# Performance work log

Hardware: AMD Instinct MI355X
Metric: run time of the kernel (lower is better)

Reference implementation:

```python
import jax, jax.numpy as jnp
import numpy as np

N, E, D, H = 50000, 800000, 128, 4
C = D // H  # per-head out channels
NEG_SLOPE = 0.2
BN_EPS = 1e-5


def _glorot(key, shape, fan):
    return jax.random.normal(key, shape, jnp.float32) / np.sqrt(fan)


def setup_inputs() -> dict:
    key = jax.random.key(0)
    ks = jax.random.split(key, 8)
    inp = {
        'x': jax.random.normal(ks[0], (N, D), jnp.float32),
        'edge_index': jax.random.randint(ks[1], (2, E), 0, N, dtype=jnp.int32),
        'Wl1': _glorot(ks[2], (D, D), D), 'Wr1': _glorot(ks[3], (D, D), D),
        'att1': _glorot(ks[4], (H, C), C), 'b1': jnp.zeros((D,), jnp.float32),
        'gamma1': jnp.ones((D,), jnp.float32), 'beta1': jnp.zeros((D,), jnp.float32),
        'Wl2': _glorot(ks[5], (D, D), D), 'Wr2': _glorot(ks[6], (D, D), D),
        'att2': _glorot(ks[7], (H, C), C), 'b2': jnp.zeros((D,), jnp.float32),
        'gamma2': jnp.ones((D,), jnp.float32), 'beta2': jnp.zeros((D,), jnp.float32),
    }
    return inp


def gatv2_conv(x, src, dst, Wl, Wr, att, bias):
    # PyG GATv2Conv, concat=True, add_self_loops handled by caller.
    n = x.shape[0]
    xl = (x @ Wl).reshape(n, H, C)  # source-side transform
    xr = (x @ Wr).reshape(n, H, C)  # target-side transform
    e = xl[src] + xr[dst]                      # [E', H, C]
    e = jnp.where(e > 0, e, NEG_SLOPE * e)     # LeakyReLU
    logits = jnp.einsum('ehc,hc->eh', e, att)  # [E', H]
    # segment softmax over destination node
    m = jax.ops.segment_max(logits, dst, num_segments=n)  # [N, H]
    ex = jnp.exp(logits - m[dst])
    den = jax.ops.segment_sum(ex, dst, num_segments=n)
    alpha = ex / den[dst]                      # [E', H]
    out = jax.ops.segment_sum(alpha[:, :, None] * xl[src], dst, num_segments=n)
    return out.reshape(n, H * C) + bias


def batchnorm(x, gamma, beta):
    mu = x.mean(0)
    var = x.var(0)
    return gamma * (x - mu) * jax.lax.rsqrt(var + BN_EPS) + beta


def reference(x, edge_index, Wl1, Wr1, att1, b1, gamma1, beta1,
              Wl2, Wr2, att2, b2, gamma2, beta2):
    n = x.shape[0]
    loop = jnp.arange(n, dtype=edge_index.dtype)
    src = jnp.concatenate([edge_index[0], loop])  # add self-loops (PyG default)
    dst = jnp.concatenate([edge_index[1], loop])
    identity = x
    out = gatv2_conv(x, src, dst, Wl1, Wr1, att1, b1)
    out = jax.nn.relu(batchnorm(out, gamma1, beta1))
    out = gatv2_conv(out, src, dst, Wl2, Wr2, att2, b2)
    out = batchnorm(out, gamma2, beta2) + identity
    return jax.nn.relu(out)
```

## Files before the change

kernel.cpp:

```cpp
#include <hip/hip_runtime.h>
#include <cstdint>
#include <cstddef>

#define D 128
#define BN_EPS 1e-5f
#define NEG_INF -3.0e38f
#define BN_BLOCKS 512

typedef __attribute__((ext_vector_type(8))) short bf16x8;
typedef __attribute__((ext_vector_type(4))) float f32x4;

static __device__ __forceinline__ unsigned short f2bf(float f) {
    uint32_t u = __float_as_uint(f);
    uint32_t r = (u + 0x7fffu + ((u >> 16) & 1u)) >> 16;
    return (unsigned short)r;
}

static __device__ __forceinline__ float qsum4(float x) {
    x += __int_as_float(__builtin_amdgcn_update_dpp(0, __float_as_int(x), 0xB1, 0xF, 0xF, true));
    x += __int_as_float(__builtin_amdgcn_update_dpp(0, __float_as_int(x), 0x4E, 0xF, 0xF, true));
    return x;
}

__global__ void zero_kernel(int* cnt, int n, unsigned short* esrc_tail) {
    int i = blockIdx.x * 256 + threadIdx.x;
    if (i < n) cnt[i] = 0;
    if (i < 16) esrc_tail[i] = 0;
}

__global__ void hist_kernel(const int* __restrict__ dst, int* __restrict__ cnt, int E) {
    int e = blockIdx.x * 256 + threadIdx.x;
    if (e < E) atomicAdd(&cnt[dst[e]], 1);
}

__global__ void scan_block(const int* __restrict__ cnt, int* __restrict__ row_start,
                           int* __restrict__ bsum, int n) {
    __shared__ int tmp[256];
    int tid = threadIdx.x;
    int i = blockIdx.x * 256 + tid;
    int v = (i < n) ? cnt[i] : 0;
    tmp[tid] = v; __syncthreads();
    for (int off = 1; off < 256; off <<= 1) {
        int t = (tid >= off) ? tmp[tid - off] : 0;
        __syncthreads();
        tmp[tid] += t; __syncthreads();
    }
    if (i < n) row_start[i + 1] = tmp[tid];
    if (tid == 255) bsum[blockIdx.x] = tmp[255];
}

__global__ void scan_bsum(int* bsum, int nb) {
    __shared__ int tmp[256];
    int tid = threadIdx.x;
    int v = (tid < nb) ? bsum[tid] : 0;
    tmp[tid] = v; __syncthreads();
    for (int off = 1; off < 256; off <<= 1) {
        int t = (tid >= off) ? tmp[tid - off] : 0;
        __syncthreads();
        tmp[tid] += t; __syncthreads();
    }
    if (tid < nb) bsum[tid] = tmp[tid];
}

__global__ void scan_fix(int* __restrict__ row_start, const int* __restrict__ bsum,
                         int* __restrict__ cursor, int n) {
    int i = blockIdx.x * 256 + threadIdx.x;
    if (i < n) {
        int add = (blockIdx.x > 0) ? bsum[blockIdx.x - 1] : 0;
        int val = row_start[i + 1] + add;
        row_start[i + 1] = val;
        if (i + 1 < n) cursor[i + 1] = val;
    }
    if (i == 0) { row_start[0] = 0; cursor[0] = 0; }
}

__global__ void scatter_kernel(const int* __restrict__ src, const int* __restrict__ dst,
                               int* __restrict__ cursor, unsigned short* __restrict__ esrc, int E) {
    int e = blockIdx.x * 256 + threadIdx.x;
    if (e < E) {
        int p = atomicAdd(&cursor[dst[e]], 1);
        esrc[p] = (unsigned short)src[e];
    }
}

__global__ void repack_w(const float* __restrict__ Wl, const float* __restrict__ Wr,
                         unsigned short* __restrict__ Bp) {
    int idx = blockIdx.x * 256 + threadIdx.x;
    int i    = idx & 7;
    int lane = (idx >> 3) & 63;
    int kt   = (idx >> 9) & 3;
    int jt   = idx >> 11;
    int k   = kt * 32 + (lane >> 4) * 8 + i;
    int col = jt * 16 + (lane & 15);
    float v = (col < 128) ? Wl[k * 128 + col] : Wr[k * 128 + (col - 128)];
    Bp[idx] = f2bf(v);
}

template<bool BN>
__global__ __launch_bounds__(256, 2) void gemm_mfma(
    const float* __restrict__ X, const unsigned short* __restrict__ Bp,
    const float* __restrict__ scale, const float* __restrict__ shift,
    unsigned short* __restrict__ xl, float* __restrict__ xr, int n)
{
    __shared__ unsigned short smem[32768];
    {
        const float4* s = (const float4*)Bp;
        float4* d = (float4*)smem;
        #pragma unroll
        for (int it = 0; it < 16; ++it)
            d[it * 256 + threadIdx.x] = s[it * 256 + threadIdx.x];
    }
    __syncthreads();

    int wid = threadIdx.x >> 6, lane = threadIdx.x & 63;
    int nw = (n + 31) >> 5;
    int wrow = blockIdx.x * 4 + wid;
    if (wrow >= nw) return;
    int r0 = wrow * 32;
    int m = lane & 15, hi = lane >> 4;

    f32x4 accA[16], accB[16];
    #pragma unroll
    for (int jt = 0; jt < 16; ++jt) {
        accA[jt] = (f32x4){0.f, 0.f, 0.f, 0.f};
        accB[jt] = (f32x4){0.f, 0.f, 0.f, 0.f};
    }

    int rA = r0 + m;      if (rA > n - 1) rA = n - 1;
    int rB = r0 + 16 + m; if (rB > n - 1) rB = n - 1;
    const float* xrowA = X + (size_t)rA * D;
    const float* xrowB = X + (size_t)rB * D;

    #pragma unroll
    for (int kt = 0; kt < 4; ++kt) {
        int kb = kt * 32 + hi * 8;
        float sca[8], shf[8];
        if (BN) {
            float4 s0 = *(const float4*)(scale + kb);
            float4 s1 = *(const float4*)(scale + kb + 4);
            float4 h0 = *(const float4*)(shift + kb);
            float4 h1 = *(const float4*)(shift + kb + 4);
            sca[0]=s0.x; sca[1]=s0.y; sca[2]=s0.z; sca[3]=s0.w;
            sca[4]=s1.x; sca[5]=s1.y; sca[6]=s1.z; sca[7]=s1.w;
            shf[0]=h0.x; shf[1]=h0.y; shf[2]=h0.z; shf[3]=h0.w;
            shf[4]=h1.x; shf[5]=h1.y; shf[6]=h1.z; shf[7]=h1.w;
        }
        float4 a0 = *(const float4*)(xrowA + kb);
        float4 a1 = *(const float4*)(xrowA + kb + 4);
        float4 b0 = *(const float4*)(xrowB + kb);
        float4 b1 = *(const float4*)(xrowB + kb + 4);
        float avA[8] = {a0.x, a0.y, a0.z, a0.w, a1.x, a1.y, a1.z, a1.w};
        float avB[8] = {b0.x, b0.y, b0.z, b0.w, b1.x, b1.y, b1.z, b1.w};
        bf16x8 afragA, afragB;
        #pragma unroll
        for (int i = 0; i < 8; ++i) {
            float va = avA[i], vb = avB[i];
            if (BN) {
                va = fmaxf(va * sca[i] + shf[i], 0.f);
                vb = fmaxf(vb * sca[i] + shf[i], 0.f);
            }
            afragA[i] = (short)f2bf(va);
            afragB[i] = (short)f2bf(vb);
        }
        #pragma unroll
        for (int jt = 0; jt < 16; ++jt) {
            bf16x8 bfrag = *(const bf16x8*)(smem + (size_t)((jt * 4 + kt) * 64 + lane) * 8);
            accA[jt] = __builtin_amdgcn_mfma_f32_16x16x32_bf16(afragA, bfrag, accA[jt], 0, 0, 0);
            accB[jt] = __builtin_amdgcn_mfma_f32_16x16x32_bf16(afragB, bfrag, accB[jt], 0, 0, 0);
        }
    }

    #pragma unroll
    for (int jt = 0; jt < 16; ++jt) {
        int col = jt * 16 + m;
        #pragma unroll
        for (int r = 0; r < 4; ++r) {
            int rowA = r0 + hi * 4 + r;
            int rowB = rowA + 16;
            if (rowA < n) {
                float v = accA[jt][r];
                if (jt < 8) xl[(size_t)rowA * D + col] = f2bf(v);
                else        xr[(size_t)rowA * D + (col - 128)] = v;
            }
            if (rowB < n) {
                float v = accB[jt][r];
                if (jt < 8) xl[(size_t)rowB * D + col] = f2bf(v);
                else        xr[(size_t)rowB * D + (col - 128)] = v;
            }
        }
    }
}

__global__ __launch_bounds__(256) void gat_kernel(
    const unsigned short* __restrict__ xl, const float* __restrict__ xr,
    const float* __restrict__ att, const float* __restrict__ bias,
    const int* __restrict__ row_start, const unsigned short* __restrict__ esrc,
    float* __restrict__ h, int n)
{
    const float L2E = 1.44269504089f;
    int wid = threadIdx.x >> 6;
    int lane = threadIdx.x & 63;
    int v = blockIdx.x * 4 + wid;
    if (v >= n) return;
    int g  = lane >> 4;
    int il = lane & 15;

    float xrv[8], av[8];
    {
        float4 xa = *(const float4*)(xr + (size_t)v * D + il * 8);
        float4 xb = *(const float4*)(xr + (size_t)v * D + il * 8 + 4);
        xrv[0]=xa.x; xrv[1]=xa.y; xrv[2]=xa.z; xrv[3]=xa.w;
        xrv[4]=xb.x; xrv[5]=xb.y; xrv[6]=xb.z; xrv[7]=xb.w;
        float4 aa = *(const float4*)(att + il * 8);
        float4 ab = *(const float4*)(att + il * 8 + 4);
        av[0]=aa.x*L2E; av[1]=aa.y*L2E; av[2]=aa.z*L2E; av[3]=aa.w*L2E;
        av[4]=ab.x*L2E; av[5]=ab.y*L2E; av[6]=ab.z*L2E; av[7]=ab.w*L2E;
    }

    int p = row_start[v];
    int deg = row_start[v + 1] - p;
    int vcnt = deg + 1;

    float m = NEG_INF, den = 0.f;
    float acc[8] = {0.f, 0.f, 0.f, 0.f, 0.f, 0.f, 0.f, 0.f};

    auto unpack = [](uint4 q, float* x) {
        x[0] = __uint_as_float(q.x << 16); x[1] = __uint_as_float(q.x & 0xffff0000u);
        x[2] = __uint_as_float(q.y << 16); x[3] = __uint_as_float(q.y & 0xffff0000u);
        x[4] = __uint_as_float(q.z << 16); x[5] = __uint_as_float(q.z & 0xffff0000u);
        x[6] = __uint_as_float(q.w << 16); x[7] = __uint_as_float(q.w & 0xffff0000u);
    };
    auto logit = [&](const float* x) {
        float d = 0.f;
        #pragma unroll
        for (int k = 0; k < 8; ++k) {
            float f = x[k] + xrv[k];
            f = fmaxf(f, 0.2f * f);
            d = fmaf(av[k], f, d);
        }
        return qsum4(d);
    };

    {
        uint32_t u0 = (g == 0) ? (uint32_t)v : (uint32_t)esrc[p + g - 1];
        bool val0 = g < vcnt;
        uint4 q0 = *(const uint4*)(xl + ((size_t)u0 << 7) + il * 8);
        float x[8]; unpack(q0, x);
        float lg = val0 ? logit(x) : NEG_INF;
        if (__any(lg > m + 8.f)) { m = fmaxf(m, lg); }
        float pex = val0 ? exp2f(lg - m) : 0.f;
        den += pex;
        #pragma unroll
        for (int k = 0; k < 8; ++k) acc[k] = fmaf(pex, x[k], acc[k]);
    }
    for (int base = 4; base < vcnt; base += 8) {
        int iA = base + g, iB = base + 4 + g;
        bool vA = iA < vcnt, vB = iB < vcnt;
        uint32_t uA = vA ? (uint32_t)esrc[p + iA - 1] : 0u;
        uint32_t uB = vB ? (uint32_t)esrc[p + iB - 1] : 0u;
        uint4 qA = *(const uint4*)(xl + ((size_t)uA << 7) + il * 8);
        uint4 qB = *(const uint4*)(xl + ((size_t)uB << 7) + il * 8);
        float xA[8], xB[8];
        unpack(qA, xA); unpack(qB, xB);
        float lgA = logit(xA); lgA = vA ? lgA : NEG_INF;
        float lgB = logit(xB); lgB = vB ? lgB : NEG_INF;
        float mx = fmaxf(lgA, lgB);
        if (__any(mx > m + 8.f)) {
            float nm = fmaxf(m, mx);
            float sc = exp2f(m - nm);
            den *= sc;
            #pragma unroll
            for (int k = 0; k < 8; ++k) acc[k] *= sc;
            m = nm;
        }
        float pA = exp2f(lgA - m);
        float pB = exp2f(lgB - m);
        den += pA + pB;
        #pragma unroll
        for (int k = 0; k < 8; ++k)
            acc[k] = fmaf(pA, xA[k], fmaf(pB, xB[k], acc[k]));
    }

    float m2 = fmaxf(m, __shfl_xor(m, 16));
    float M  = fmaxf(m2, __shfl_xor(m2, 32));
    float sc = exp2f(m - M);
    den *= sc;
    den += __shfl_xor(den, 16);
    den += __shfl_xor(den, 32);
    #pragma unroll
    for (int k = 0; k < 8; ++k) {
        acc[k] *= sc;
        acc[k] += __shfl_xor(acc[k], 16);
        acc[k] += __shfl_xor(acc[k], 32);
    }
    if (g == 0) {
        float inv = 1.f / den;
        float4 ba = *(const float4*)(bias + il * 8);
        float4 bb = *(const float4*)(bias + il * 8 + 4);
        float4 o0, o1;
        o0.x = fmaf(acc[0], inv, ba.x); o0.y = fmaf(acc[1], inv, ba.y);
        o0.z = fmaf(acc[2], inv, ba.z); o0.w = fmaf(acc[3], inv, ba.w);
        o1.x = fmaf(acc[4], inv, bb.x); o1.y = fmaf(acc[5], inv, bb.y);
        o1.z = fmaf(acc[6], inv, bb.z); o1.w = fmaf(acc[7], inv, bb.w);
        *(float4*)(h + (size_t)v * D + il * 8)     = o0;
        *(float4*)(h + (size_t)v * D + il * 8 + 4) = o1;
    }
}

__global__ __launch_bounds__(256) void bn_stats(const float* __restrict__ h,
                                                float* __restrict__ psum, float* __restrict__ psum2, int n)
{
    int c4 = threadIdx.x & 31;
    int ty = threadIdx.x >> 5;
    float sx = 0.f, sy = 0.f, sz = 0.f, sw = 0.f;
    float qx = 0.f, qy = 0.f, qz = 0.f, qw = 0.f;
    for (int r = blockIdx.x * 8 + ty; r < n; r += gridDim.x * 8) {
        float4 v = *(const float4*)(h + (size_t)r * D + c4 * 4);
        sx += v.x; sy += v.y; sz += v.z; sw += v.w;
        qx = fmaf(v.x, v.x, qx); qy = fmaf(v.y, v.y, qy);
        qz = fmaf(v.z, v.z, qz); qw = fmaf(v.w, v.w, qw);
    }
    __shared__ float4 smA[256], smB[256];
    smA[threadIdx.x] = make_float4(sx, sy, sz, sw);
    smB[threadIdx.x] = make_float4(qx, qy, qz, qw);
    __syncthreads();
    #pragma unroll
    for (int off = 128; off >= 32; off >>= 1) {
        if (threadIdx.x < off) {
            float4 a = smA[threadIdx.x], b = smA[threadIdx.x + off];
            smA[threadIdx.x] = make_float4(a.x + b.x, a.y + b.y, a.z + b.z, a.w + b.w);
            float4 c = smB[threadIdx.x], d2 = smB[threadIdx.x + off];
            smB[threadIdx.x] = make_float4(c.x + d2.x, c.y + d2.y, c.z + d2.z, c.w + d2.w);
        }
        __syncthreads();
    }
    if (threadIdx.x < 32) {
        ((float4*)psum)[blockIdx.x * 32 + threadIdx.x]  = smA[threadIdx.x];
        ((float4*)psum2)[blockIdx.x * 32 + threadIdx.x] = smB[threadIdx.x];
    }
}

__global__ __launch_bounds__(256) void bn_mid(const float* __restrict__ psum, const float* __restrict__ psum2,
                                              float* __restrict__ pmid, float* __restrict__ pmid2)
{
    int c4 = threadIdx.x & 31;
    int rg = threadIdx.x >> 5;
    float4 s = make_float4(0.f, 0.f, 0.f, 0.f), q = make_float4(0.f, 0.f, 0.f, 0.f);
    #pragma unroll
    for (int k = 0; k < 4; ++k) {
        int r = blockIdx.x * 32 + rg + k * 8;
        float4 a = ((const float4*)psum)[r * 32 + c4];
        float4 b = ((const float4*)psum2)[r * 32 + c4];
        s.x += a.x; s.y += a.y; s.z += a.z; s.w += a.w;
        q.x += b.x; q.y += b.y; q.z += b.z; q.w += b.w;
    }
    __shared__ float4 smA[256], smB[256];
    smA[threadIdx.x] = s; smB[threadIdx.x] = q;
    __syncthreads();
    #pragma unroll
    for (int off = 128; off >= 32; off >>= 1) {
        if (threadIdx.x < off) {
            float4 a = smA[threadIdx.x], b = smA[threadIdx.x + off];
            smA[threadIdx.x] = make_float4(a.x + b.x, a.y + b.y, a.z + b.z, a.w + b.w);
            float4 c = smB[threadIdx.x], d2 = smB[threadIdx.x + off];
            smB[threadIdx.x] = make_float4(c.x + d2.x, c.y + d2.y, c.z + d2.z, c.w + d2.w);
        }
        __syncthreads();
    }
    if (threadIdx.x < 32) {
        ((float4*)pmid)[blockIdx.x * 32 + threadIdx.x]  = smA[threadIdx.x];
        ((float4*)pmid2)[blockIdx.x * 32 + threadIdx.x] = smB[threadIdx.x];
    }
}

__global__ void bn_final(const float* __restrict__ psum, const float* __restrict__ psum2,
                         const float* __restrict__ gamma, const float* __restrict__ beta,
                         float* __restrict__ scale, float* __restrict__ shift,
                         float inv_n, int nblk)
{
    int c = threadIdx.x & 127;
    int half = threadIdx.x >> 7;
    float s = 0.f, s2 = 0.f;
    for (int b = half; b < nblk; b += 2) {
        s  += psum[b * 128 + c];
        s2 += psum2[b * 128 + c];
    }
    __shared__ float sm[256], sm2[256];
    sm[threadIdx.x] = s; sm2[threadIdx.x] = s2; __syncthreads();
    if (half == 0) {
        s  += sm[threadIdx.x + 128];
        s2 += sm2[threadIdx.x + 128];
        float mu = s * inv_n;
        float var = s2 * inv_n - mu * mu;
        float inv = rsqrtf(var + BN_EPS);
        float sc = gamma[c] * inv;
        scale[c] = sc;
        shift[c] = beta[c] - mu * sc;
    }
}

__global__ __launch_bounds__(256) void final_kernel(
    const float* __restrict__ h2, const float* __restrict__ x,
    const float* __restrict__ scale, const float* __restrict__ shift,
    float* __restrict__ out, int total)
{
    int i = blockIdx.x * 256 + threadIdx.x;
    if (i * 4 >= total) return;
    float4 hv = ((const float4*)h2)[i];
    float4 xv = ((const float4*)x)[i];
    int c = (i * 4) & 127;
    float4 o;
    o.x = fmaxf(hv.x * scale[c + 0] + shift[c + 0] + xv.x, 0.f);
    o.y = fmaxf(hv.y * scale[c + 1] + shift[c + 1] + xv.y, 0.f);
    o.z = fmaxf(hv.z * scale[c + 2] + shift[c + 2] + xv.z, 0.f);
    o.w = fmaxf(hv.w * scale[c + 3] + shift[c + 3] + xv.w, 0.f);
    ((float4*)out)[i] = o;
}

extern "C" void kernel_launch(void* const* d_in, const int* in_sizes, int n_in,
                              void* d_out, int out_size, void* d_ws, size_t ws_size,
                              hipStream_t stream)
{
    const float* x    = (const float*)d_in[0];
    const int*   ei   = (const int*)  d_in[1];
    const float* Wl1  = (const float*)d_in[2];
    const float* Wr1  = (const float*)d_in[3];
    const float* att1 = (const float*)d_in[4];
    const float* b1   = (const float*)d_in[5];
    const float* g1   = (const float*)d_in[6];
    const float* be1  = (const float*)d_in[7];
    const float* Wl2  = (const float*)d_in[8];
    const float* Wr2  = (const float*)d_in[9];
    const float* att2 = (const float*)d_in[10];
    const float* b2   = (const float*)d_in[11];
    const float* g2   = (const float*)d_in[12];
    const float* be2  = (const float*)d_in[13];
    float* out = (float*)d_out;

    int n = in_sizes[0] / D;
    int E = in_sizes[1] / 2;
    const int* e_src = ei;
    const int* e_dst = ei + E;

    char* w = (char*)d_ws;
    auto alloc = [&](size_t bytes) -> char* {
        char* p = w;
        w += (bytes + 255) / 256 * 256;
        return p;
    };
    unsigned short* xl = (unsigned short*)alloc((size_t)n * D * 2);
    float* xr          = (float*)alloc((size_t)n * D * 4);
    float* h           = (float*)alloc((size_t)n * D * 4);
    int* row_start     = (int*)alloc((size_t)(n + 1) * 4);
    int* cnt           = (int*)alloc((size_t)n * 4);
    int* cursor        = (int*)alloc((size_t)n * 4);
    unsigned short* esrc = (unsigned short*)alloc((size_t)(E + 16) * 2);
    int* bsum          = (int*)alloc(256 * 4);
    float* bn          = (float*)alloc(4 * 128 * 4);
    float* psum        = (float*)alloc((size_t)BN_BLOCKS * 128 * 4);
    float* psum2       = (float*)alloc((size_t)BN_BLOCKS * 128 * 4);
    float* pmid        = (float*)alloc(16 * 128 * 4);
    float* pmid2       = (float*)alloc(16 * 128 * 4);
    unsigned short* Bp1 = (unsigned short*)alloc(32768 * 2);
    unsigned short* Bp2 = (unsigned short*)alloc(32768 * 2);

    int nb = (n + 255) / 256;
    int gemm_blocks = (((n + 31) / 32) + 3) / 4;

    zero_kernel<<<(n + 255) / 256, 256, 0, stream>>>(cnt, n, esrc + E);
    hist_kernel<<<(E + 255) / 256, 256, 0, stream>>>(e_dst, cnt, E);
    scan_block<<<nb, 256, 0, stream>>>(cnt, row_start, bsum, n);
    scan_bsum<<<1, 256, 0, stream>>>(bsum, nb);
    scan_fix<<<nb, 256, 0, stream>>>(row_start, bsum, cursor, n);
    scatter_kernel<<<(E + 255) / 256, 256, 0, stream>>>(e_src, e_dst, cursor, esrc, E);
    repack_w<<<128, 256, 0, stream>>>(Wl1, Wr1, Bp1);
    repack_w<<<128, 256, 0, stream>>>(Wl2, Wr2, Bp2);

    gemm_mfma<false><<<gemm_blocks, 256, 0, stream>>>(x, Bp1, nullptr, nullptr, xl, xr, n);
    gat_kernel<<<(n + 3) / 4, 256, 0, stream>>>(xl, xr, att1, b1, row_start, esrc, h, n);
    bn_stats<<<BN_BLOCKS, 256, 0, stream>>>(h, psum, psum2, n);
    bn_mid<<<16, 256, 0, stream>>>(psum, psum2, pmid, pmid2);
    bn_final<<<1, 256, 0, stream>>>(pmid, pmid2, g1, be1, bn + 0, bn + 128, 1.0f / n, 16);

    gemm_mfma<true><<<gemm_blocks, 256, 0, stream>>>(h, Bp2, bn + 0, bn + 128, xl, xr, n);
    gat_kernel<<<(n + 3) / 4, 256, 0, stream>>>(xl, xr, att2, b2, row_start, esrc, h, n);
    bn_stats<<<BN_BLOCKS, 256, 0, stream>>>(h, psum, psum2, n);
    bn_mid<<<16, 256, 0, stream>>>(psum, psum2, pmid, pmid2);
    bn_final<<<1, 256, 0, stream>>>(pmid, pmid2, g2, be2, bn + 256, bn + 384, 1.0f / n, 16);

    final_kernel<<<((n * D / 4) + 255) / 256, 256, 0, stream>>>(h, x, bn + 256, bn + 384, out, n * D);
}
```

Before: 265.6 us.

## Fold self-loops into CSR, merge BN reduction and repack kernels, simplify LeakyReLU

Self-loops are now written into the CSR edge list during the scan, so the GAT kernel no longer has a separate peeled first iteration and drops the per-edge validity select on index loads. LeakyReLU is rewritten algebraically as 0.6*f + 0.4*|f|, with the attention weights prescaled. The two-stage BN reduction (bn_mid + bn_final) is collapsed into a single kernel with fewer partial blocks, and the two weight repacks are merged into one launch. The aim is to cut launch count and per-edge instruction overhead, at the cost of a larger esrc buffer and less parallelism in the BN statistics pass.

Result: no change. 267.1 us (median of 2 runs) (+0.6%).

```diff
diff --git a/kernel.cpp b/kernel.cpp
--- a/kernel.cpp
+++ b/kernel.cpp
@@ -5,7 +5,8 @@
 #define D 128
 #define BN_EPS 1e-5f
 #define NEG_INF -3.0e38f
-#define BN_BLOCKS 512
+#define M_INIT  -1.0e30f
+#define BN_BLOCKS 128
 
 typedef __attribute__((ext_vector_type(8))) short bf16x8;
 typedef __attribute__((ext_vector_type(4))) float f32x4;
@@ -24,7 +25,7 @@
 
 __global__ void zero_kernel(int* cnt, int n, unsigned short* esrc_tail) {
     int i = blockIdx.x * 256 + threadIdx.x;
-    if (i < n) cnt[i] = 0;
+    if (i < n) cnt[i] = 1;
     if (i < 16) esrc_tail[i] = 0;
 }
 
@@ -63,15 +64,18 @@
 }
 
 __global__ void scan_fix(int* __restrict__ row_start, const int* __restrict__ bsum,
-                         int* __restrict__ cursor, int n) {
+                         int* __restrict__ cursor, unsigned short* __restrict__ esrc, int n) {
     int i = blockIdx.x * 256 + threadIdx.x;
     if (i < n) {
         int add = (blockIdx.x > 0) ? bsum[blockIdx.x - 1] : 0;
         int val = row_start[i + 1] + add;
         row_start[i + 1] = val;
-        if (i + 1 < n) cursor[i + 1] = val;
-    }
-    if (i == 0) { row_start[0] = 0; cursor[0] = 0; }
+        if (i + 1 < n) {
+            cursor[i + 1] = val + 1;
+            esrc[val] = (unsigned short)(i + 1);
+        }
+    }
+    if (i == 0) { row_start[0] = 0; cursor[0] = 1; esrc[0] = 0; }
 }
 
 __global__ void scatter_kernel(const int* __restrict__ src, const int* __restrict__ dst,
@@ -83,9 +87,15 @@
     }
 }
 
-__global__ void repack_w(const float* __restrict__ Wl, const float* __restrict__ Wr,
-                         unsigned short* __restrict__ Bp) {
-    int idx = blockIdx.x * 256 + threadIdx.x;
+__global__ void repack_w2(const float* __restrict__ Wl1, const float* __restrict__ Wr1,
+                          const float* __restrict__ Wl2, const float* __restrict__ Wr2,
+                          unsigned short* __restrict__ Bp1, unsigned short* __restrict__ Bp2) {
+    int gid = blockIdx.x;
+    bool second = gid >= 128;
+    int idx = (second ? gid - 128 : gid) * 256 + threadIdx.x;
+    const float* Wl = second ? Wl2 : Wl1;
+    const float* Wr = second ? Wr2 : Wr1;
+    unsigned short* Bp = second ? Bp2 : Bp1;
     int i    = idx & 7;
     int lane = (idx >> 3) & 63;
     int kt   = (idx >> 9) & 3;
@@ -205,7 +215,7 @@
     int g  = lane >> 4;
     int il = lane & 15;
 
-    float xrv[8], av[8];
+    float xrv[8], a06[8], a04[8];
     {
         float4 xa = *(const float4*)(xr + (size_t)v * D + il * 8);
         float4 xb = *(const float4*)(xr + (size_t)v * D + il * 8 + 4);
@@ -213,15 +223,18 @@
         xrv[4]=xb.x; xrv[5]=xb.y; xrv[6]=xb.z; xrv[7]=xb.w;
         float4 aa = *(const float4*)(att + il * 8);
         float4 ab = *(const float4*)(att + il * 8 + 4);
-        av[0]=aa.x*L2E; av[1]=aa.y*L2E; av[2]=aa.z*L2E; av[3]=aa.w*L2E;
-        av[4]=ab.x*L2E; av[5]=ab.y*L2E; av[6]=ab.z*L2E; av[7]=ab.w*L2E;
+        float t[8] = {aa.x, aa.y, aa.z, aa.w, ab.x, ab.y, ab.z, ab.w};
+        #pragma unroll
+        for (int k = 0; k < 8; ++k) {
+            a06[k] = 0.6f * L2E * t[k];
+            a04[k] = 0.4f * L2E * t[k];
+        }
     }
 
     int p = row_start[v];
-    int deg = row_start[v + 1] - p;
-    int vcnt = deg + 1;
-
-    float m = NEG_INF, den = 0.f;
+    int vcnt = row_start[v + 1] - p;
+
+    float m = M_INIT, den = 0.f;
     float acc[8] = {0.f, 0.f, 0.f, 0.f, 0.f, 0.f, 0.f, 0.f};
 
     auto unpack = [](uint4 q, float* x) {
@@ -231,33 +244,21 @@
         x[6] = __uint_as_float(q.w << 16); x[7] = __uint_as_float(q.w & 0xffff0000u);
     };
     auto logit = [&](const float* x) {
-        float d = 0.f;
+        float d0 = 0.f, d1 = 0.f;
         #pragma unroll
         for (int k = 0; k < 8; ++k) {
             float f = x[k] + xrv[k];
-            f = fmaxf(f, 0.2f * f);
-            d = fmaf(av[k], f, d);
-        }
-        return qsum4(d);
+            d0 = fmaf(a06[k], f, d0);
+            d1 = fmaf(a04[k], fabsf(f), d1);
+        }
+        return qsum4(d0 + d1);
     };
 
-    {
-        uint32_t u0 = (g == 0) ? (uint32_t)v : (uint32_t)esrc[p + g - 1];
-        bool val0 = g < vcnt;
-        uint4 q0 = *(const uint4*)(xl + ((size_t)u0 << 7) + il * 8);
-        float x[8]; unpack(q0, x);
-        float lg = val0 ? logit(x) : NEG_INF;
-        if (__any(lg > m + 8.f)) { m = fmaxf(m, lg); }
-        float pex = val0 ? exp2f(lg - m) : 0.f;
-        den += pex;
-        #pragma unroll
-        for (int k = 0; k < 8; ++k) acc[k] = fmaf(pex, x[k], acc[k]);
-    }
-    for (int base = 4; base < vcnt; base += 8) {
-        int iA = base + g, iB = base + 4 + g;
+    for (int base = 0; base < vcnt; base += 8) {
+        int iA = base + g, iB = iA + 4;
         bool vA = iA < vcnt, vB = iB < vcnt;
-        uint32_t uA = vA ? (uint32_t)esrc[p + iA - 1] : 0u;
-        uint32_t uB = vB ? (uint32_t)esrc[p + iB - 1] : 0u;
+        uint32_t uA = (uint32_t)esrc[p + iA];
+        uint32_t uB = (uint32_t)esrc[p + iB];
         uint4 qA = *(const uint4*)(xl + ((size_t)uA << 7) + il * 8);
         uint4 qB = *(const uint4*)(xl + ((size_t)uB << 7) + il * 8);
         float xA[8], xB[8];
@@ -340,15 +341,15 @@
     }
 }
 
-__global__ __launch_bounds__(256) void bn_mid(const float* __restrict__ psum, const float* __restrict__ psum2,
-                                              float* __restrict__ pmid, float* __restrict__ pmid2)
+__global__ __launch_bounds__(256) void bn_final(
+    const float* __restrict__ psum, const float* __restrict__ psum2,
+    const float* __restrict__ gamma, const float* __restrict__ beta,
+    float* __restrict__ scale, float* __restrict__ shift, float inv_n, int nblk)
 {
     int c4 = threadIdx.x & 31;
     int rg = threadIdx.x >> 5;
     float4 s = make_float4(0.f, 0.f, 0.f, 0.f), q = make_float4(0.f, 0.f, 0.f, 0.f);
-    #pragma unroll
-    for (int k = 0; k < 4; ++k) {
-        int r = blockIdx.x * 32 + rg + k * 8;
+    for (int r = rg; r < nblk; r += 8) {
         float4 a = ((const float4*)psum)[r * 32 + c4];
         float4 b = ((const float4*)psum2)[r * 32 + c4];
         s.x += a.x; s.y += a.y; s.z += a.z; s.w += a.w;
@@ -368,34 +369,28 @@
         __syncthreads();
     }
     if (threadIdx.x < 32) {
-        ((float4*)pmid)[blockIdx.x * 32 + threadIdx.x]  = smA[threadIdx.x];
-        ((float4*)pmid2)[blockIdx.x * 32 + threadIdx.x] = smB[threadIdx.x];
-    }
-}
-
-__global__ void bn_final(const float* __restrict__ psum, const float* __restrict__ psum2,
-                         const float* __restrict__ gamma, const float* __restrict__ beta,
-                         float* __restrict__ scale, float* __restrict__ shift,
-                         float inv_n, int nblk)
-{
-    int c = threadIdx.x & 127;
-    int half = threadIdx.x >> 7;
-    float s = 0.f, s2 = 0.f;
-    for (int b = half; b < nblk; b += 2) {
-        s  += psum[b * 128 + c];
-        s2 += psum2[b * 128 + c];
-    }
-    __shared__ float sm[256], sm2[256];
-    sm[threadIdx.x] = s; sm2[threadIdx.x] = s2; __syncthreads();
-    if (half == 0) {
-        s  += sm[threadIdx.x + 128];
-        s2 += sm2[threadIdx.x + 128];
-        float mu = s * inv_n;
-        float var = s2 * inv_n - mu * mu;
-        float inv = rsqrtf(var + BN_EPS);
-        float sc = gamma[c] * inv;
-        scale[c] = sc;
-        shift[c] = beta[c] - mu * sc;
+        float4 S = smA[threadIdx.x], Q = smB[threadIdx.x];
+        float4 ga = ((const float4*)gamma)[threadIdx.x];
+        float4 be = ((const float4*)beta)[threadIdx.x];
+        float4 sc, sh;
+        {
+            float mu = S.x * inv_n, var = Q.x * inv_n - mu * mu;
+            float iv = rsqrtf(var + BN_EPS); sc.x = ga.x * iv; sh.x = be.x - mu * sc.x;
+        }
+        {
+            float mu = S.y * inv_n, var = Q.y * inv_n - mu * mu;
+            float iv = rsqrtf(var + BN_EPS); sc.y = ga.y * iv; sh.y = be.y - mu * sc.y;
+        }
+        {
+            float mu = S.z * inv_n, var = Q.z * inv_n - mu * mu;
+            float iv = rsqrtf(var + BN_EPS); sc.z = ga.z * iv; sh.z = be.z - mu * sc.z;
+        }
+        {
+            float mu = S.w * inv_n, var = Q.w * inv_n - mu * mu;
+            float iv = rsqrtf(var + BN_EPS); sc.w = ga.w * iv; sh.w = be.w - mu * sc.w;
+        }
+        ((float4*)scale)[threadIdx.x] = sc;
+        ((float4*)shift)[threadIdx.x] = sh;
     }
 }
 
@@ -454,39 +449,34 @@
     int* row_start     = (int*)alloc((size_t)(n + 1) * 4);
     int* cnt           = (int*)alloc((size_t)n * 4);
     int* cursor        = (int*)alloc((size_t)n * 4);
-    unsigned short* esrc = (unsigned short*)alloc((size_t)(E + 16) * 2);
+    unsigned short* esrc = (unsigned short*)alloc((size_t)(E + n + 16) * 2);
     int* bsum          = (int*)alloc(256 * 4);
     float* bn          = (float*)alloc(4 * 128 * 4);
     float* psum        = (float*)alloc((size_t)BN_BLOCKS * 128 * 4);
     float* psum2       = (float*)alloc((size_t)BN_BLOCKS * 128 * 4);
-    float* pmid        = (float*)alloc(16 * 128 * 4);
-    float* pmid2       = (float*)alloc(16 * 128 * 4);
     unsigned short* Bp1 = (unsigned short*)alloc(32768 * 2);
     unsigned short* Bp2 = (unsigned short*)alloc(32768 * 2);
 
     int nb = (n + 255) / 256;
     int gemm_blocks = (((n + 31) / 32) + 3) / 4;
 
-    zero_kernel<<<(n + 255) / 256, 256, 0, stream>>>(cnt, n, esrc + E);
+    zero_kernel<<<nb, 256, 0, stream>>>(cnt, n, esrc + E + n);
     hist_kernel<<<(E + 255) / 256, 256, 0, stream>>>(e_dst, cnt, E);
     scan_block<<<nb, 256, 0, stream>>>(cnt, row_start, bsum, n);
     scan_bsum<<<1, 256, 0, stream>>>(bsum, nb);
-    scan_fix<<<nb, 256, 0, stream>>>(row_start, bsum, cursor, n);
+    scan_fix<<<nb, 256, 0, stream>>>(row_start, bsum, cursor, esrc, n);
     scatter_kernel<<<(E + 255) / 256, 256, 0, stream>>>(e_src, e_dst, cursor, esrc, E);
-    repack_w<<<128, 256, 0, stream>>>(Wl1, Wr1, Bp1);
-    repack_w<<<128, 256, 0, stream>>>(Wl2, Wr2, Bp2);
+    repack_w2<<<256, 256, 0, stream>>>(Wl1, Wr1, Wl2, Wr2, Bp1, Bp2);
 
     gemm_mfma<false><<<gemm_blocks, 256, 0, stream>>>(x, Bp1, nullptr, nullptr, xl, xr, n);
     gat_kernel<<<(n + 3) / 4, 256, 0, stream>>>(xl, xr, att1, b1, row_start, esrc, h, n);
     bn_stats<<<BN_BLOCKS, 256, 0, stream>>>(h, psum, psum2, n);
-    bn_mid<<<16, 256, 0, stream>>>(psum, psum2, pmid, pmid2);
-    bn_final<<<1, 256, 0, stream>>>(pmid, pmid2, g1, be1, bn + 0, bn + 128, 1.0f / n, 16);
+    bn_final<<<1, 256, 0, stream>>>(psum, psum2, g1, be1, bn + 0, bn + 128, 1.0f / n, BN_BLOCKS);
 
     gemm_mfma<true><<<gemm_blocks, 256, 0, stream>>>(h, Bp2, bn + 0, bn + 128, xl, xr, n);
     gat_kernel<<<(n + 3) / 4, 256, 0, stream>>>(xl, xr, att2, b2, row_start, esrc, h, n);
     bn_stats<<<BN_BLOCKS, 256, 0, stream>>>(h, psum, psum2, n);
-    bn_mid<<<16, 256, 0, stream>>>(psum, psum2, pmid, pmid2);
-    bn_final<<<1, 256, 0, stream>>>(pmid, pmid2, g2, be2, bn + 256, bn + 384, 1.0f / n, 16);
+    bn_final<<<1, 256, 0, stream>>>(psum, psum2, g2, be2, bn + 256, bn + 384, 1.0f / n, BN_BLOCKS);
 
     final_kernel<<<((n * D / 4) + 255) / 256, 256, 0, stream>>>(h, x, bn + 256, bn + 384, out, n * D);
 }
```
